# Optimization experiments

Hardware: AMD Instinct MI355X
Metric: run time of the kernel (lower is better)

Reference implementation:

```python
import jax, jax.numpy as jnp
import numpy as np

B, T, D, N, K, H = 2, 2048, 3584, 16, 8, 256
WINDOW = 1024
SOFT_CAP = 50.0
SCALAR = 0.0625  # head_dim ** -0.5
BASE = 10000.0
K_MASK = -2.3819763e38


def apply_rope(x, pos):
    # x: [B, S, heads, H], pos: [B, S]
    frac = 2.0 * jnp.arange(H // 2, dtype=jnp.float32) / H
    timescale = BASE ** frac  # [H/2]
    sinusoid = pos[..., None].astype(jnp.float32) / timescale  # [B, S, H/2]
    sinusoid = sinusoid[..., None, :]  # [B, S, 1, H/2]
    sin, cos = jnp.sin(sinusoid), jnp.cos(sinusoid)
    first, second = jnp.split(x, 2, axis=-1)
    out = jnp.concatenate([first * cos - second * sin,
                           second * cos + first * sin], axis=-1)
    return out.astype(x.dtype)


def setup_inputs() -> dict:
    key = jax.random.key(0)
    ks = jax.random.split(key, 4)
    x = jax.random.normal(ks[0], (B, T, D), jnp.float32)
    q_w = jax.random.normal(ks[1], (N, D, H), jnp.float32) * 0.02
    kv_w = jax.random.normal(ks[2], (2, K, D, H), jnp.float32) * 0.02
    o_w = jax.random.normal(ks[3], (N, H, D), jnp.float32) * 0.02
    segment_pos = jnp.broadcast_to(jnp.arange(T, dtype=jnp.int32), (B, T))
    attn_mask = jnp.tril(jnp.ones((1, T, T), dtype=bool))  # causal [#B, T, S]
    return {"x": x, "segment_pos": segment_pos, "attn_mask": attn_mask,
            "q_w": q_w, "kv_w": kv_w, "o_w": o_w}


def reference(x, segment_pos, attn_mask, q_w, kv_w, o_w):
    # Projections (GQA path: num_kv_heads != num_heads)
    q = jnp.einsum('BTD,NDH->BTNH', x, q_w)
    kv = jnp.einsum('BSD,CKDH->CBSKH', x, kv_w)
    k, v = kv[0], kv[1]
    # RoPE on keys and queries, then query scaling
    k = apply_rope(k, segment_pos)
    q = apply_rope(q, segment_pos) * SCALAR
    # GQA: group N query heads over K kv heads
    G = N // K
    qg = q.reshape(B, T, K, G, H)
    logits = jnp.einsum('BTKGH,BSKH->BTKGS', qg, k).reshape(B, T, N, T)
    # Logit soft cap
    logits = jnp.tanh(logits / SOFT_CAP) * SOFT_CAP
    # Sliding-window causal mask (attn_mask is causal, S > window)
    mask = jnp.triu(attn_mask, 1 - WINDOW)  # [#B, T, S]
    padded = jnp.where(mask[:, :, None, :], logits, K_MASK)
    probs = jax.nn.softmax(padded, axis=-1).astype(k.dtype)
    enc = jnp.einsum('BTKGS,BSKH->BTKGH', probs.reshape(B, T, K, G, T), v)
    enc = enc.reshape(B, T, N, H)
    out = jnp.einsum('BTNH,NHD->BTD', enc, o_w)
    no_attended = jnp.all(mask == 0, axis=-1, keepdims=True)  # [#B, T, 1]
    return jnp.where(no_attended, jnp.zeros_like(out), out)
```

## Files before the change

kernel.cpp:

```cpp
#include <hip/hip_runtime.h>
#include <stdint.h>


typedef short bf16x8 __attribute__((ext_vector_type(8)));
typedef float f32x4 __attribute__((ext_vector_type(4)));

#define MFMA16(a, b, c) __builtin_amdgcn_mfma_f32_16x16x32_bf16((a), (b), (c), 0, 0, 0)

__device__ __forceinline__ uint16_t f2bf(float f) {
  uint32_t u = __builtin_bit_cast(uint32_t, f);
  u += 0x7FFFu + ((u >> 16) & 1u);
  return (uint16_t)(u >> 16);
}
__device__ __forceinline__ float bf2f(uint16_t u) {
  return __builtin_bit_cast(float, (uint32_t)u << 16);
}
__device__ __forceinline__ void async16(void* lds, const void* g) {
  __builtin_amdgcn_global_load_lds(
      (const __attribute__((address_space(1))) uint32_t*)g,
      (__attribute__((address_space(3))) uint32_t*)lds, 16, 0, 0);
}

__global__ void convert_x(const float* __restrict__ x, uint16_t* __restrict__ xb) {
  size_t i = ((size_t)blockIdx.x * 256 + threadIdx.x) * 8;
  f32x4 a = *(const f32x4*)(x + i);
  f32x4 b = *(const f32x4*)(x + i + 4);
  bf16x8 r;
  r[0] = (short)f2bf(a[0]); r[1] = (short)f2bf(a[1]);
  r[2] = (short)f2bf(a[2]); r[3] = (short)f2bf(a[3]);
  r[4] = (short)f2bf(b[0]); r[5] = (short)f2bf(b[1]);
  r[6] = (short)f2bf(b[2]); r[7] = (short)f2bf(b[3]);
  *(bf16x8*)(xb + i) = r;
}

__global__ void transpose_qkvw(const float* __restrict__ qw,
                               const float* __restrict__ kvw,
                               uint16_t* __restrict__ WqkvT) {
  __shared__ uint16_t tile[64][65];
  const int j0 = blockIdx.x * 64;
  const int d0 = blockIdx.y * 64;
  const int t = threadIdx.x;
  const int jl = t & 63;
  const int q4 = t >> 6;
  const int j = j0 + jl;
  const float* src;
  if (j0 < 4096) {
    src = qw + (size_t)(j >> 8) * 3584 * 256 + (j & 255);
  } else {
    int j2 = j - 4096;
    src = kvw + ((size_t)((j2 >> 11) * 8 + ((j2 >> 8) & 7)) * 3584) * 256 + (j2 & 255);
  }
#pragma unroll
  for (int r = 0; r < 16; ++r) {
    int dl = r * 4 + q4;
    tile[jl][dl] = f2bf(src[(size_t)(d0 + dl) * 256]);
  }
  __syncthreads();
#pragma unroll
  for (int r = 0; r < 16; ++r) {
    int jl2 = r * 4 + q4;
    WqkvT[(size_t)(j0 + jl2) * 3584 + d0 + jl] = tile[jl2][jl];
  }
}

__global__ void transpose_ow(const float* __restrict__ ow, uint16_t* __restrict__ WoT) {
  __shared__ uint16_t tile[64][65];
  const int d0 = blockIdx.x * 64;
  const int j0 = blockIdx.y * 64;
  const int t = threadIdx.x;
  const int c = t & 63;
  const int q4 = t >> 6;
#pragma unroll
  for (int r = 0; r < 16; ++r) {
    int jl = r * 4 + q4;
    tile[c][jl] = f2bf(ow[(size_t)(j0 + jl) * 3584 + d0 + c]);
  }
  __syncthreads();
#pragma unroll
  for (int r = 0; r < 16; ++r) {
    int dl = r * 4 + q4;
    WoT[(size_t)(d0 + dl) * 4096 + j0 + c] = tile[dl][c];
  }
}

template <int EPI>
__global__ __launch_bounds__(512, 2) void gemm256(
    const uint16_t* __restrict__ A, const uint16_t* __restrict__ Bt,
    int Kd, int Nc, int nbx,
    void* __restrict__ Oqv, uint16_t* __restrict__ Ok, uint16_t* __restrict__ Ov) {
  __shared__ uint16_t lds[4 * 16384];

  const int tid = threadIdx.x;
  const int lane = tid & 63;
  const int quad = lane >> 4;
  const int l15 = lane & 15;
  const int wave = tid >> 6;
  const int wm = wave & 1;
  const int wn = wave >> 1;

  const int nwg = gridDim.x;
  const int chunk = nwg >> 3;
  const int wg = blockIdx.x;
  const int swz = (wg & 7) * chunk + (wg >> 3);
  const int by = swz / nbx;
  const int bx = swz - by * nbx;
  const int m0 = by * 256;
  const int n0 = bx * 256;

  f32x4 acc[8][4];
#pragma unroll
  for (int i = 0; i < 8; ++i)
#pragma unroll
    for (int j = 0; j < 4; ++j) acc[i][j] = f32x4{0.f, 0.f, 0.f, 0.f};

  const int srow = tid >> 2;
  const int sck = tid & 3;
  const int gck0 = sck ^ ((srow >> 1) & 3);
  const int gck1 = sck ^ (((srow + 128) >> 1) & 3);
  const uint16_t* gA0 = A + (size_t)(m0 + srow) * Kd + gck0 * 8;
  const uint16_t* gA1 = A + (size_t)(m0 + srow + 128) * Kd + gck1 * 8;
  const uint16_t* gB0 = Bt + (size_t)(n0 + srow) * Kd + gck0 * 8;
  const uint16_t* gB1 = Bt + (size_t)(n0 + srow + 128) * Kd + gck1 * 8;

  const int T = Kd >> 5;

#pragma unroll
  for (int pt = 0; pt < 3; ++pt) {
    uint16_t* sd = lds + pt * 16384;
    const int kt = pt * 32;
    async16(sd + tid * 8, gA0 + kt);
    async16(sd + 4096 + tid * 8, gA1 + kt);
    async16(sd + 8192 + tid * 8, gB0 + kt);
    async16(sd + 12288 + tid * 8, gB1 + kt);
  }
  asm volatile("s_waitcnt vmcnt(8)" ::: "memory");
  __builtin_amdgcn_s_barrier();

  const int arow = wm * 128;
  const int brow = wn * 64;

  for (int t = 0; t < T; ++t) {
    const uint16_t* sA = lds + (t & 3) * 16384;
    const uint16_t* sB = sA + 8192;
    uint16_t* sd = lds + ((t + 3) & 3) * 16384;
    int ts = t + 3;
    if (ts >= T) ts = T - 1;
    const int ktS = ts * 32;

    bf16x8 bfr[4], af[4];
#pragma unroll
    for (int fn = 0; fn < 4; ++fn) {
      const int r = brow + fn * 16 + l15;
      bfr[fn] = *(const bf16x8*)(sB + r * 32 + ((quad ^ ((r >> 1) & 3)) << 3));
    }
#pragma unroll
    for (int i = 0; i < 4; ++i) {
      const int r = arow + i * 16 + l15;
      af[i] = *(const bf16x8*)(sA + r * 32 + ((quad ^ ((r >> 1) & 3)) << 3));
    }
    async16(sd + tid * 8, gA0 + ktS);
    async16(sd + 4096 + tid * 8, gA1 + ktS);
    __builtin_amdgcn_s_barrier();
    __builtin_amdgcn_s_setprio(1);
#pragma unroll
    for (int i = 0; i < 4; ++i)
#pragma unroll
      for (int fn = 0; fn < 4; ++fn)
        acc[i][fn] = MFMA16(af[i], bfr[fn], acc[i][fn]);
    __builtin_amdgcn_s_setprio(0);
    __builtin_amdgcn_s_barrier();

#pragma unroll
    for (int i = 0; i < 4; ++i) {
      const int r = arow + 64 + i * 16 + l15;
      af[i] = *(const bf16x8*)(sA + r * 32 + ((quad ^ ((r >> 1) & 3)) << 3));
    }
    async16(sd + 8192 + tid * 8, gB0 + ktS);
    async16(sd + 12288 + tid * 8, gB1 + ktS);
    asm volatile("s_waitcnt vmcnt(8)" ::: "memory");
    __builtin_amdgcn_s_barrier();
    __builtin_amdgcn_s_setprio(1);
#pragma unroll
    for (int i = 0; i < 4; ++i)
#pragma unroll
      for (int fn = 0; fn < 4; ++fn)
        acc[4 + i][fn] = MFMA16(af[i], bfr[fn], acc[4 + i][fn]);
    __builtin_amdgcn_s_setprio(0);
    __builtin_amdgcn_s_barrier();
  }

  asm volatile("s_waitcnt vmcnt(0)" ::: "memory");

  const int rowb = m0 + wm * 128;
  const int colb = n0 + wn * 64;
  if (EPI == 0) {
    if (n0 < 4096) {
      uint16_t* Oq = (uint16_t*)Oqv;
#pragma unroll
      for (int fm = 0; fm < 8; ++fm)
#pragma unroll
        for (int fn = 0; fn < 4; ++fn) {
          const int r0 = rowb + fm * 16 + quad * 4;
          const int c = colb + fn * 16 + l15;
#pragma unroll
          for (int reg = 0; reg < 4; ++reg)
            Oq[(size_t)(r0 + reg) * 4096 + c] = f2bf(acc[fm][fn][reg]);
        }
    } else if (n0 < 6144) {
#pragma unroll
      for (int fm = 0; fm < 8; ++fm)
#pragma unroll
        for (int fn = 0; fn < 4; ++fn) {
          const int r0 = rowb + fm * 16 + quad * 4;
          const int c = colb + fn * 16 + l15 - 4096;
#pragma unroll
          for (int reg = 0; reg < 4; ++reg)
            Ok[(size_t)(r0 + reg) * 2048 + c] = f2bf(acc[fm][fn][reg]);
        }
    } else {
#pragma unroll
      for (int fm = 0; fm < 8; ++fm)
#pragma unroll
        for (int fn = 0; fn < 4; ++fn) {
          const int r0 = rowb + fm * 16 + quad * 4;
          const int c2 = colb + fn * 16 + l15 - 6144;
          const int kvh = c2 >> 8, h = c2 & 255;
          const int bb = r0 >> 11, tt = r0 & 2047;
          ushort4 pk;
          pk.x = f2bf(acc[fm][fn][0]);
          pk.y = f2bf(acc[fm][fn][1]);
          pk.z = f2bf(acc[fm][fn][2]);
          pk.w = f2bf(acc[fm][fn][3]);
          *(ushort4*)(Ov + ((((size_t)bb * 8 + kvh) * 256 + h) * 2048 + tt)) = pk;
        }
    }
  } else {
    float* Oq = (float*)Oqv;
#pragma unroll
    for (int fm = 0; fm < 8; ++fm)
#pragma unroll
      for (int fn = 0; fn < 4; ++fn) {
        const int r0 = rowb + fm * 16 + quad * 4;
        const int c = colb + fn * 16 + l15;
#pragma unroll
        for (int reg = 0; reg < 4; ++reg)
          Oq[(size_t)(r0 + reg) * Nc + c] = acc[fm][fn][reg];
      }
  }
}

__global__ void rope_kernel(uint16_t* __restrict__ Qb, uint16_t* __restrict__ Kb,
                            const int* __restrict__ segpos) {
  const size_t QN = (size_t)2 * 2048 * 16 * 128;
  size_t idx = (size_t)blockIdx.x * 256 + threadIdx.x;
  uint16_t* buf;
  size_t base;
  int i, t, b;
  bool isQ = idx < QN;
  if (isQ) {
    i = (int)(idx & 127);
    int nn = (int)((idx >> 7) & 15);
    t = (int)((idx >> 11) & 2047);
    b = (int)(idx >> 22);
    base = ((size_t)((b * 2048 + t) * 16 + nn) << 8) + i;
    buf = Qb;
  } else {
    size_t x2 = idx - QN;
    i = (int)(x2 & 127);
    int kh = (int)((x2 >> 7) & 7);
    t = (int)((x2 >> 10) & 2047);
    b = (int)(x2 >> 21);
    base = ((size_t)((b * 2048 + t) * 8 + kh) << 8) + i;
    buf = Kb;
  }
  float pos = (float)segpos[b * 2048 + t];
  float inv = exp2f((float)i * (-13.287712379549449f / 128.f));
  float ang = pos * inv;
  float sn = sinf(ang), cs = cosf(ang);
  float x1 = bf2f(buf[base]);
  float x2v = bf2f(buf[base + 128]);
  float o1 = x1 * cs - x2v * sn;
  float o2 = x2v * cs + x1 * sn;
  if (isQ) { o1 *= 0.0625f; o2 *= 0.0625f; }
  buf[base] = f2bf(o1);
  buf[base + 128] = f2bf(o2);
}

__global__ __launch_bounds__(256) void attn_kernel(
    const uint16_t* __restrict__ Qb, const uint16_t* __restrict__ Kb,
    const uint16_t* __restrict__ Vt, uint16_t* __restrict__ enc) {
  __shared__ uint16_t KV[256 * 72];
  __shared__ uint16_t Ps[4 * 32 * 72];
  const int tid = threadIdx.x;
  const int lane = tid & 63;
  const int wave = tid >> 6;
  const int quad = lane >> 4;
  const int l15 = lane & 15;
  const int qt0 = blockIdx.x * 64;
  const int b = blockIdx.y >> 3;
  const int kvh = blockIdx.y & 7;
  const int g = wave & 1;
  const int wr = (wave >> 1) * 32;
  const int n = kvh * 2 + g;

  f32x4 oacc[2][16];
#pragma unroll
  for (int mt = 0; mt < 2; ++mt)
#pragma unroll
    for (int ht = 0; ht < 16; ++ht) oacc[mt][ht] = f32x4{0.f, 0.f, 0.f, 0.f};
  float mrow[2][4], lrow[2][4];
#pragma unroll
  for (int mt = 0; mt < 2; ++mt)
#pragma unroll
    for (int r = 0; r < 4; ++r) { mrow[mt][r] = -50.f; lrow[mt][r] = 0.f; }

  const uint16_t* qp0 =
      Qb + ((size_t)((b * 2048 + qt0 + wr + l15) * 16 + n) << 8) + quad * 8;
  const uint16_t* qp1 = qp0 + (size_t)16 * 4096;

  const int krow = tid >> 5;
  const int kcol = (tid & 31) * 8;
  const uint16_t* kg = Kb + ((size_t)((b * 2048 + krow) * 8 + kvh) << 8) + kcol;
  const int vrow = tid >> 3;
  const int vcol = (tid & 7) * 8;
  const uint16_t* vg = Vt + (((size_t)(b * 8 + kvh) * 256 + vrow) << 11) + vcol;

  int lo = qt0 - 1023;
  if (lo < 0) lo = 0;
  const int s0_start = (lo >> 6) << 6;

  for (int s0 = s0_start; s0 <= qt0; s0 += 64) {
    bf16x8 kr[8], vr[8];
#pragma unroll
    for (int r = 0; r < 8; ++r) {
      kr[r] = *(const bf16x8*)(kg + (size_t)(s0 + r * 8) * 2048);
      vr[r] = *(const bf16x8*)(vg + s0 + (size_t)(r * 32) * 2048);
    }
    __syncthreads();
#pragma unroll
    for (int r = 0; r < 8; ++r)
      *(bf16x8*)(KV + (r * 8 + krow) * 264 + kcol) = kr[r];
    __syncthreads();

    f32x4 sac[2][4];
#pragma unroll
    for (int mt = 0; mt < 2; ++mt)
#pragma unroll
      for (int j = 0; j < 4; ++j) sac[mt][j] = f32x4{0.f, 0.f, 0.f, 0.f};
#pragma unroll
    for (int c = 0; c < 8; ++c) {
      bf16x8 q0 = *(const bf16x8*)(qp0 + c * 32);
      bf16x8 q1 = *(const bf16x8*)(qp1 + c * 32);
#pragma unroll
      for (int j = 0; j < 4; ++j) {
        bf16x8 kf = *(const bf16x8*)(KV + (j * 16 + l15) * 264 + (c * 4 + quad) * 8);
        sac[0][j] = MFMA16(q0, kf, sac[0][j]);
        sac[1][j] = MFMA16(q1, kf, sac[1][j]);
      }
    }

#pragma unroll
    for (int mt = 0; mt < 2; ++mt) {
      const int tbase = qt0 + wr + mt * 16 + quad * 4;
#pragma unroll
      for (int reg = 0; reg < 4; ++reg) {
        const int t = tbase + reg;
        float pv[4];
        float mx = -1e30f;
#pragma unroll
        for (int j = 0; j < 4; ++j) {
          int s = s0 + j * 16 + l15;
          float v = sac[mt][j][reg];
          float e = __expf(v * 0.04f);
          float scv = 50.f - 100.f / (e + 1.f);
          bool valid = (s <= t) && (s + 1024 > t);
          v = valid ? scv : -1e30f;
          pv[j] = v;
          mx = fmaxf(mx, v);
        }
        mx = fmaxf(mx, __shfl_xor(mx, 1));
        mx = fmaxf(mx, __shfl_xor(mx, 2));
        mx = fmaxf(mx, __shfl_xor(mx, 4));
        mx = fmaxf(mx, __shfl_xor(mx, 8));
        float mold = mrow[mt][reg];
        float mnew = fmaxf(mold, mx);
        mrow[mt][reg] = mnew;
        float alpha = __expf(mold - mnew);
        float rs = 0.f;
#pragma unroll
        for (int j = 0; j < 4; ++j) {
          float p = __expf(pv[j] - mnew);
          pv[j] = p;
          rs += p;
        }
        rs += __shfl_xor(rs, 1);
        rs += __shfl_xor(rs, 2);
        rs += __shfl_xor(rs, 4);
        rs += __shfl_xor(rs, 8);
        lrow[mt][reg] = lrow[mt][reg] * alpha + rs;
#pragma unroll
        for (int ht = 0; ht < 16; ++ht) oacc[mt][ht][reg] *= alpha;
        const int r = mt * 16 + quad * 4 + reg;
#pragma unroll
        for (int j = 0; j < 4; ++j)
          Ps[wave * 2304 + r * 72 + j * 16 + l15] = f2bf(pv[j]);
      }
    }
    __syncthreads();
#pragma unroll
    for (int r = 0; r < 8; ++r)
      *(bf16x8*)(KV + (r * 32 + vrow) * 72 + vcol) = vr[r];
    __syncthreads();

#pragma unroll
    for (int c2 = 0; c2 < 2; ++c2) {
      const int lch = c2 * 4 + quad;
      bf16x8 pf0 = *(const bf16x8*)(Ps + wave * 2304 + l15 * 72 + lch * 8);
      bf16x8 pf1 = *(const bf16x8*)(Ps + wave * 2304 + (16 + l15) * 72 + lch * 8);
#pragma unroll
      for (int ht = 0; ht < 16; ++ht) {
        bf16x8 vf = *(const bf16x8*)(KV + (ht * 16 + l15) * 72 + lch * 8);
        oacc[0][ht] = MFMA16(pf0, vf, oacc[0][ht]);
        oacc[1][ht] = MFMA16(pf1, vf, oacc[1][ht]);
      }
    }
  }

#pragma unroll
  for (int mt = 0; mt < 2; ++mt) {
    const int tb = qt0 + wr + mt * 16 + quad * 4;
#pragma unroll
    for (int reg = 0; reg < 4; ++reg) {
      float li = 1.f / lrow[mt][reg];
      size_t base = ((size_t)((b * 2048 + tb + reg) * 16 + n) << 8) + l15;
#pragma unroll
      for (int ht = 0; ht < 16; ++ht)
        enc[base + ht * 16] = f2bf(oacc[mt][ht][reg] * li);
    }
  }
}

extern "C" void kernel_launch(void* const* d_in, const int* in_sizes, int n_in,
                              void* d_out, int out_size, void* d_ws, size_t ws_size,
                              hipStream_t stream) {
  const float* x = (const float*)d_in[0];
  const int* segpos = (const int*)d_in[1];
  const float* qw = (const float*)d_in[3];
  const float* kvw = (const float*)d_in[4];
  const float* ow = (const float*)d_in[5];
  float* out = (float*)d_out;

  uint16_t* ws = (uint16_t*)d_ws;
  uint16_t* WqkvT = ws;
  uint16_t* enc = ws;
  uint16_t* xb = ws + (size_t)29360128;
  uint16_t* WoT = ws + (size_t)29360128;
  uint16_t* Qb = ws + (size_t)44040192;
  uint16_t* Kb = ws + (size_t)60817408;
  uint16_t* Vt = ws + (size_t)69206016;

  convert_x<<<7168, 256, 0, stream>>>(x, xb);
  transpose_qkvw<<<dim3(128, 56), 256, 0, stream>>>(qw, kvw, WqkvT);
  gemm256<0><<<dim3(512), dim3(512), 0, stream>>>(xb, WqkvT, 3584, 8192, 32, Qb, Kb, Vt);
  rope_kernel<<<49152, 256, 0, stream>>>(Qb, Kb, segpos);
  attn_kernel<<<dim3(32, 16), 256, 0, stream>>>(Qb, Kb, Vt, enc);
  transpose_ow<<<dim3(56, 64), 256, 0, stream>>>(ow, WoT);
  gemm256<1><<<dim3(224), dim3(512), 0, stream>>>(enc, WoT, 4096, 3584, 14, out, nullptr, nullptr);
}
```

Before: 831.3 us.

## Restructure attention kernel with async K prefetch, smaller q tiles, lazy rescale

Rewrites the attention kernel so each block handles 32 query rows instead of 64, launched as a 1D swizzled grid of 1024 blocks with launch bounds for three blocks per CU. K tiles are staged into an XOR-swizzled LDS buffer with async global-to-LDS loads that are prefetched for the next step during softmax, while V is read directly from global memory instead of through LDS. It also skips the online-softmax rescale unless the running max grows by more than a threshold, and raises wave priority around the MFMA loops. The aims are better occupancy and load balance and less exposed load latency, at the cost of uncached global V reads and more redundant K/V traffic across the smaller blocks.

```diff
diff --git a/kernel.cpp b/kernel.cpp
--- a/kernel.cpp
+++ b/kernel.cpp
@@ -286,157 +286,152 @@
   buf[base + 128] = f2bf(o2);
 }
 
-__global__ __launch_bounds__(256) void attn_kernel(
+__device__ __forceinline__ void stage_k(uint16_t* Ks, const uint16_t* kge,
+                                        const uint16_t* kgo, int tid, int s0) {
+#pragma unroll
+  for (int r = 0; r < 8; ++r) {
+    const uint16_t* src = ((r & 1) ? kgo : kge) + (size_t)(s0 + r * 8) * 2048;
+    async16(Ks + r * 2048 + tid * 8, src);
+  }
+}
+
+__global__ __launch_bounds__(256, 3) void attn_kernel(
     const uint16_t* __restrict__ Qb, const uint16_t* __restrict__ Kb,
     const uint16_t* __restrict__ Vt, uint16_t* __restrict__ enc) {
-  __shared__ uint16_t KV[256 * 72];
-  __shared__ uint16_t Ps[4 * 32 * 72];
+  __shared__ uint16_t Ks[64 * 256];
+  __shared__ uint16_t Ps[4 * 16 * 72];
   const int tid = threadIdx.x;
   const int lane = tid & 63;
   const int wave = tid >> 6;
   const int quad = lane >> 4;
   const int l15 = lane & 15;
-  const int qt0 = blockIdx.x * 64;
-  const int b = blockIdx.y >> 3;
-  const int kvh = blockIdx.y & 7;
+
+  const int bid = blockIdx.x;
+  const int swz = (bid & 7) * 128 + (bid >> 3);
+  const int qt0 = (swz & 63) * 32;
+  const int y = swz >> 6;
+  const int b = y >> 3;
+  const int kvh = y & 7;
   const int g = wave & 1;
-  const int wr = (wave >> 1) * 32;
+  const int wr = (wave >> 1) * 16;
   const int n = kvh * 2 + g;
 
-  f32x4 oacc[2][16];
-#pragma unroll
-  for (int mt = 0; mt < 2; ++mt)
-#pragma unroll
-    for (int ht = 0; ht < 16; ++ht) oacc[mt][ht] = f32x4{0.f, 0.f, 0.f, 0.f};
-  float mrow[2][4], lrow[2][4];
-#pragma unroll
-  for (int mt = 0; mt < 2; ++mt)
-#pragma unroll
-    for (int r = 0; r < 4; ++r) { mrow[mt][r] = -50.f; lrow[mt][r] = 0.f; }
-
-  const uint16_t* qp0 =
+  f32x4 oacc[16];
+#pragma unroll
+  for (int ht = 0; ht < 16; ++ht) oacc[ht] = f32x4{0.f, 0.f, 0.f, 0.f};
+  float mrow[4], lrow[4];
+#pragma unroll
+  for (int r = 0; r < 4; ++r) { mrow[r] = -50.f; lrow[r] = 0.f; }
+
+  const uint16_t* qp =
       Qb + ((size_t)((b * 2048 + qt0 + wr + l15) * 16 + n) << 8) + quad * 8;
-  const uint16_t* qp1 = qp0 + (size_t)16 * 4096;
-
-  const int krow = tid >> 5;
-  const int kcol = (tid & 31) * 8;
-  const uint16_t* kg = Kb + ((size_t)((b * 2048 + krow) * 8 + kvh) << 8) + kcol;
-  const int vrow = tid >> 3;
-  const int vcol = (tid & 7) * 8;
-  const uint16_t* vg = Vt + (((size_t)(b * 8 + kvh) * 256 + vrow) << 11) + vcol;
+
+  const int srow8 = tid >> 5;
+  const int schunk = tid & 31;
+  const uint16_t* kgb = Kb + (size_t)b * 4194304 + kvh * 256;
+  const uint16_t* kge = kgb + srow8 * 2048 + ((schunk ^ srow8) << 3);
+  const uint16_t* kgo = kgb + srow8 * 2048 + ((schunk ^ srow8 ^ 8) << 3);
+
+  const uint16_t* vgb = Vt + ((size_t)(b * 8 + kvh) << 19);
 
   int lo = qt0 - 1023;
   if (lo < 0) lo = 0;
   const int s0_start = (lo >> 6) << 6;
 
+  stage_k(Ks, kge, kgo, tid, s0_start);
+  __syncthreads();
+
   for (int s0 = s0_start; s0 <= qt0; s0 += 64) {
-    bf16x8 kr[8], vr[8];
-#pragma unroll
-    for (int r = 0; r < 8; ++r) {
-      kr[r] = *(const bf16x8*)(kg + (size_t)(s0 + r * 8) * 2048);
-      vr[r] = *(const bf16x8*)(vg + s0 + (size_t)(r * 32) * 2048);
-    }
+    f32x4 sac[4];
+#pragma unroll
+    for (int j = 0; j < 4; ++j) sac[j] = f32x4{0.f, 0.f, 0.f, 0.f};
+    __builtin_amdgcn_s_setprio(1);
+#pragma unroll
+    for (int c = 0; c < 8; ++c) {
+      bf16x8 q0 = *(const bf16x8*)(qp + c * 32);
+#pragma unroll
+      for (int j = 0; j < 4; ++j) {
+        bf16x8 kf = *(const bf16x8*)(Ks + (j * 16 + l15) * 256 +
+                                     (((c * 4 + quad) ^ l15) << 3));
+        sac[j] = MFMA16(q0, kf, sac[j]);
+      }
+    }
+    __builtin_amdgcn_s_setprio(0);
     __syncthreads();
-#pragma unroll
-    for (int r = 0; r < 8; ++r)
-      *(bf16x8*)(KV + (r * 8 + krow) * 264 + kcol) = kr[r];
-    __syncthreads();
-
-    f32x4 sac[2][4];
-#pragma unroll
-    for (int mt = 0; mt < 2; ++mt)
-#pragma unroll
-      for (int j = 0; j < 4; ++j) sac[mt][j] = f32x4{0.f, 0.f, 0.f, 0.f};
-#pragma unroll
-    for (int c = 0; c < 8; ++c) {
-      bf16x8 q0 = *(const bf16x8*)(qp0 + c * 32);
-      bf16x8 q1 = *(const bf16x8*)(qp1 + c * 32);
+    if (s0 + 64 <= qt0) stage_k(Ks, kge, kgo, tid, s0 + 64);
+
+#pragma unroll
+    for (int reg = 0; reg < 4; ++reg) {
+      const int t = qt0 + wr + quad * 4 + reg;
+      float pv[4];
+      float mx = -1e30f;
 #pragma unroll
       for (int j = 0; j < 4; ++j) {
-        bf16x8 kf = *(const bf16x8*)(KV + (j * 16 + l15) * 264 + (c * 4 + quad) * 8);
-        sac[0][j] = MFMA16(q0, kf, sac[0][j]);
-        sac[1][j] = MFMA16(q1, kf, sac[1][j]);
-      }
-    }
-
-#pragma unroll
-    for (int mt = 0; mt < 2; ++mt) {
-      const int tbase = qt0 + wr + mt * 16 + quad * 4;
-#pragma unroll
-      for (int reg = 0; reg < 4; ++reg) {
-        const int t = tbase + reg;
-        float pv[4];
-        float mx = -1e30f;
-#pragma unroll
-        for (int j = 0; j < 4; ++j) {
-          int s = s0 + j * 16 + l15;
-          float v = sac[mt][j][reg];
-          float e = __expf(v * 0.04f);
-          float scv = 50.f - 100.f / (e + 1.f);
-          bool valid = (s <= t) && (s + 1024 > t);
-          v = valid ? scv : -1e30f;
-          pv[j] = v;
-          mx = fmaxf(mx, v);
-        }
-        mx = fmaxf(mx, __shfl_xor(mx, 1));
-        mx = fmaxf(mx, __shfl_xor(mx, 2));
-        mx = fmaxf(mx, __shfl_xor(mx, 4));
-        mx = fmaxf(mx, __shfl_xor(mx, 8));
-        float mold = mrow[mt][reg];
+        int s = s0 + j * 16 + l15;
+        float v = sac[j][reg];
+        float e = __expf(v * 0.04f);
+        float scv = 50.f - 100.f / (e + 1.f);
+        bool valid = (s <= t) && (s + 1024 > t);
+        v = valid ? scv : -1e30f;
+        pv[j] = v;
+        mx = fmaxf(mx, v);
+      }
+      mx = fmaxf(mx, __shfl_xor(mx, 1));
+      mx = fmaxf(mx, __shfl_xor(mx, 2));
+      mx = fmaxf(mx, __shfl_xor(mx, 4));
+      mx = fmaxf(mx, __shfl_xor(mx, 8));
+      float mold = mrow[reg];
+      if (!__all(mx <= mold + 8.f)) {
         float mnew = fmaxf(mold, mx);
-        mrow[mt][reg] = mnew;
         float alpha = __expf(mold - mnew);
-        float rs = 0.f;
-#pragma unroll
-        for (int j = 0; j < 4; ++j) {
-          float p = __expf(pv[j] - mnew);
-          pv[j] = p;
-          rs += p;
-        }
-        rs += __shfl_xor(rs, 1);
-        rs += __shfl_xor(rs, 2);
-        rs += __shfl_xor(rs, 4);
-        rs += __shfl_xor(rs, 8);
-        lrow[mt][reg] = lrow[mt][reg] * alpha + rs;
-#pragma unroll
-        for (int ht = 0; ht < 16; ++ht) oacc[mt][ht][reg] *= alpha;
-        const int r = mt * 16 + quad * 4 + reg;
-#pragma unroll
-        for (int j = 0; j < 4; ++j)
-          Ps[wave * 2304 + r * 72 + j * 16 + l15] = f2bf(pv[j]);
-      }
-    }
-    __syncthreads();
-#pragma unroll
-    for (int r = 0; r < 8; ++r)
-      *(bf16x8*)(KV + (r * 32 + vrow) * 72 + vcol) = vr[r];
-    __syncthreads();
-
+        lrow[reg] *= alpha;
+#pragma unroll
+        for (int ht = 0; ht < 16; ++ht) oacc[ht][reg] *= alpha;
+        mrow[reg] = mnew;
+        mold = mnew;
+      }
+      float rs = 0.f;
+#pragma unroll
+      for (int j = 0; j < 4; ++j) {
+        float p = __expf(pv[j] - mold);
+        pv[j] = p;
+        rs += p;
+      }
+      rs += __shfl_xor(rs, 1);
+      rs += __shfl_xor(rs, 2);
+      rs += __shfl_xor(rs, 4);
+      rs += __shfl_xor(rs, 8);
+      lrow[reg] += rs;
+      const int r = quad * 4 + reg;
+#pragma unroll
+      for (int j = 0; j < 4; ++j)
+        Ps[wave * 1152 + r * 72 + j * 16 + l15] = f2bf(pv[j]);
+    }
+
+    __builtin_amdgcn_s_setprio(1);
 #pragma unroll
     for (int c2 = 0; c2 < 2; ++c2) {
       const int lch = c2 * 4 + quad;
-      bf16x8 pf0 = *(const bf16x8*)(Ps + wave * 2304 + l15 * 72 + lch * 8);
-      bf16x8 pf1 = *(const bf16x8*)(Ps + wave * 2304 + (16 + l15) * 72 + lch * 8);
+      bf16x8 pf = *(const bf16x8*)(Ps + wave * 1152 + l15 * 72 + lch * 8);
 #pragma unroll
       for (int ht = 0; ht < 16; ++ht) {
-        bf16x8 vf = *(const bf16x8*)(KV + (ht * 16 + l15) * 72 + lch * 8);
-        oacc[0][ht] = MFMA16(pf0, vf, oacc[0][ht]);
-        oacc[1][ht] = MFMA16(pf1, vf, oacc[1][ht]);
-      }
-    }
-  }
-
-#pragma unroll
-  for (int mt = 0; mt < 2; ++mt) {
-    const int tb = qt0 + wr + mt * 16 + quad * 4;
-#pragma unroll
-    for (int reg = 0; reg < 4; ++reg) {
-      float li = 1.f / lrow[mt][reg];
-      size_t base = ((size_t)((b * 2048 + tb + reg) * 16 + n) << 8) + l15;
-#pragma unroll
-      for (int ht = 0; ht < 16; ++ht)
-        enc[base + ht * 16] = f2bf(oacc[mt][ht][reg] * li);
-    }
+        bf16x8 vf = *(const bf16x8*)(vgb + (size_t)(ht * 16 + l15) * 2048 +
+                                     s0 + lch * 8);
+        oacc[ht] = MFMA16(pf, vf, oacc[ht]);
+      }
+    }
+    __builtin_amdgcn_s_setprio(0);
+    __syncthreads();
+  }
+
+#pragma unroll
+  for (int reg = 0; reg < 4; ++reg) {
+    float li = 1.f / lrow[reg];
+    const int t = qt0 + wr + quad * 4 + reg;
+    size_t base = ((size_t)((b * 2048 + t) * 16 + n) << 8) + l15;
+#pragma unroll
+    for (int ht = 0; ht < 16; ++ht)
+      enc[base + ht * 16] = f2bf(oacc[ht][reg] * li);
   }
 }
 
@@ -463,7 +458,7 @@
   transpose_qkvw<<<dim3(128, 56), 256, 0, stream>>>(qw, kvw, WqkvT);
   gemm256<0><<<dim3(512), dim3(512), 0, stream>>>(xb, WqkvT, 3584, 8192, 32, Qb, Kb, Vt);
   rope_kernel<<<49152, 256, 0, stream>>>(Qb, Kb, segpos);
-  attn_kernel<<<dim3(32, 16), 256, 0, stream>>>(Qb, Kb, Vt, enc);
+  attn_kernel<<<dim3(1024), 256, 0, stream>>>(Qb, Kb, Vt, enc);
   transpose_ow<<<dim3(56, 64), 256, 0, stream>>>(ow, WoT);
   gemm256<1><<<dim3(224), dim3(512), 0, stream>>>(enc, WoT, 4096, 3584, 14, out, nullptr, nullptr);
 }
```

Result: slower. 922.8 us (+11.0%).
